# Performance work log

Hardware: AMD Instinct MI355X
Metric: run time of the kernel (lower is better)

Reference implementation:

```python
import jax, jax.numpy as jnp
import numpy as np

NPOINT = 1024
RADIUS = 0.2
NSAMPLE = 32


def furthest_point_sampling(xyz, npoint):
    # xyz: (B, N, 3) -> (B, npoint) int32 indices
    B, N, _ = xyz.shape

    def step(carry, _):
        dist, far = carry
        centroid = jnp.take_along_axis(xyz, far[:, None, None], axis=1)  # (B,1,3)
        d = jnp.sum((xyz - centroid) ** 2, axis=-1)                       # (B,N)
        dist = jnp.minimum(dist, d)
        new_far = jnp.argmax(dist, axis=-1).astype(jnp.int32)
        return (dist, new_far), far

    init = (jnp.full((B, N), 1e10, xyz.dtype), jnp.zeros((B,), jnp.int32))
    _, idx = jax.lax.scan(step, init, None, length=npoint)
    return idx.T  # (B, npoint)


def ball_query(xyz, new_xyz, radius, nsample):
    # xyz: (B,N,3), new_xyz: (B,S,3) -> (B,S,nsample) int32 indices
    N = xyz.shape[1]
    d2 = jnp.sum((new_xyz[:, :, None, :] - xyz[:, None, :, :]) ** 2, axis=-1)  # (B,S,N)
    # pick first `nsample` indices within radius (CUDA ball_query semantics)
    key = jnp.where(d2 < radius * radius, jnp.arange(N, dtype=jnp.int32)[None, None, :], N)
    idx = jnp.sort(key, axis=-1)[..., :nsample]          # (B,S,nsample)
    first = idx[..., :1]
    idx = jnp.where(idx == N, first, idx)                # pad with first valid
    return jnp.clip(idx, 0, N - 1).astype(jnp.int32)     # guard empty balls


def sa_forward(xyz, features, W1, s1, b1, W2, s2, b2, W3, s3, b3):
    B, N, _ = xyz.shape
    center_idx = furthest_point_sampling(xyz, NPOINT)                     # (B,S)
    new_xyz = jnp.take_along_axis(xyz, center_idx[..., None], axis=1)     # (B,S,3)

    idx = ball_query(xyz, new_xyz, RADIUS, NSAMPLE)                       # (B,S,K)
    # group xyz (relative coords) and features
    g_xyz = jnp.take_along_axis(xyz[:, None], idx[..., None], axis=2)     # (B,S,K,3)
    g_xyz = g_xyz - new_xyz[:, :, None, :]
    feats_n = jnp.swapaxes(features, 1, 2)                                # (B,N,C)
    g_feat = jnp.take_along_axis(feats_n[:, None], idx[..., None], axis=2)  # (B,S,K,C)
    g = jnp.concatenate([g_xyz, g_feat], axis=-1)                         # (B,S,K,3+C)
    x = jnp.transpose(g, (0, 3, 1, 2))                                    # (B,3+C,S,K)

    # 1x1 conv MLP with (folded) BN affine + ReLU
    for W, s, b in ((W1, s1, b1), (W2, s2, b2), (W3, s3, b3)):
        x = jax.nn.relu(jnp.einsum('oi,bisk->bosk', W, x)
                        * s[None, :, None, None] + b[None, :, None, None])
    new_features = jnp.max(x, axis=-1)                                    # (B,Cout,S)
    return new_xyz, new_features


def setup_inputs() -> dict:
    key = jax.random.key(0)
    ks = jax.random.split(key, 11)
    B, N, C = 4, 16384, 64
    return {
        'xyz': jax.random.uniform(ks[0], (B, N, 3), jnp.float32),
        'features': jax.random.normal(ks[1], (B, C, N), jnp.float32),
        'W1': jax.random.normal(ks[2], (64, C + 3), jnp.float32) * 0.1,
        's1': jax.random.uniform(ks[3], (64,), jnp.float32),
        'b1': jax.random.normal(ks[4], (64,), jnp.float32) * 0.1,
        'W2': jax.random.normal(ks[5], (64, 64), jnp.float32) * 0.1,
        's2': jax.random.uniform(ks[6], (64,), jnp.float32),
        'b2': jax.random.normal(ks[7], (64,), jnp.float32) * 0.1,
        'W3': jax.random.normal(ks[8], (128, 64), jnp.float32) * 0.1,
        's3': jax.random.uniform(ks[9], (128,), jnp.float32),
        'b3': jax.random.normal(ks[10], (128,), jnp.float32) * 0.1,
    }


def reference(xyz, features, W1, s1, b1, W2, s2, b2, W3, s3, b3):
    return sa_forward(xyz, features, W1, s1, b1, W2, s2, b2, W3, s3, b3)
```

## Files before the change

kernel.cpp:

```cpp
#include <hip/hip_runtime.h>
#include <cstdint>
#include <cstddef>

#define BATCH   4
#define NPTS    16384
#define NPOINT  1024
#define NSAMPLE 32
#define CIN     67
#define R2f     0.04f

__global__ __launch_bounds__(1024) void fps_kernel(
    const float* __restrict__ xyz, float* __restrict__ out_newxyz)
{
  const int b = blockIdx.x;
  const float* base = xyz + (size_t)b * NPTS * 3;
  const int t = threadIdx.x;
  const int lane = t & 63, wid = t >> 6;

  float px[16], py[16], pz[16], dist[16];
#pragma unroll
  for (int j = 0; j < 16; ++j) {
    int p = t + (j << 10);
    px[j] = base[p * 3 + 0];
    py[j] = base[p * 3 + 1];
    pz[j] = base[p * 3 + 2];
    dist[j] = 1e10f;
  }

  __shared__ float s_v[16];
  __shared__ int   s_i[16];
  __shared__ int   s_far;

  int far = 0;
  float cx = base[0], cy = base[1], cz = base[2];

  for (int it = 0; it < NPOINT; ++it) {
    if (t == 0) {
      int o = (b * NPOINT + it) * 3;
      out_newxyz[o + 0] = cx;
      out_newxyz[o + 1] = cy;
      out_newxyz[o + 2] = cz;
    }
    float bv = -1.0f; int bi = 0x7fffffff;
#pragma unroll
    for (int j = 0; j < 16; ++j) {
      float dx = __fsub_rn(px[j], cx);
      float dy = __fsub_rn(py[j], cy);
      float dz = __fsub_rn(pz[j], cz);
      float d  = __fadd_rn(__fadd_rn(__fmul_rn(dx, dx), __fmul_rn(dy, dy)),
                           __fmul_rn(dz, dz));
      float nd = fminf(dist[j], d);
      dist[j] = nd;
      bool tk = nd > bv;
      bv = tk ? nd : bv;
      bi = tk ? (t + (j << 10)) : bi;
    }
#pragma unroll
    for (int off = 32; off >= 1; off >>= 1) {
      float ov = __shfl_xor(bv, off);
      int   oi = __shfl_xor(bi, off);
      bool tk = (ov > bv) || (ov == bv && oi < bi);
      bv = tk ? ov : bv;
      bi = tk ? oi : bi;
    }
    if (lane == 0) { s_v[wid] = bv; s_i[wid] = bi; }
    __syncthreads();
    if (wid == 0) {
      float v = (lane < 16) ? s_v[lane] : -1.0f;
      int   i = (lane < 16) ? s_i[lane] : 0x7fffffff;
#pragma unroll
      for (int off = 8; off >= 1; off >>= 1) {
        float ov = __shfl_xor(v, off);
        int   oi = __shfl_xor(i, off);
        bool tk = (ov > v) || (ov == v && oi < i);
        v = tk ? ov : v;
        i = tk ? oi : i;
      }
      if (lane == 0) s_far = i;
    }
    __syncthreads();
    far = s_far;
    cx = base[far * 3 + 0];
    cy = base[far * 3 + 1];
    cz = base[far * 3 + 2];
  }
}

__global__ __launch_bounds__(256) void transpose_kernel(
    const float* __restrict__ f, float* __restrict__ ft)
{
  __shared__ float tile[64][65];
  int b  = blockIdx.x >> 8;
  int n0 = (blockIdx.x & 255) << 6;
  for (int v = threadIdx.x; v < 64 * 64; v += 256) {
    int c = v >> 6, j = v & 63;
    tile[c][j] = f[((size_t)(b * 64 + c)) * NPTS + n0 + j];
  }
  __syncthreads();
  for (int v = threadIdx.x; v < 64 * 64; v += 256) {
    int j = v >> 6, c = v & 63;
    ft[((size_t)(b * NPTS + n0 + j)) * 64 + c] = tile[c][j];
  }
}

__global__ __launch_bounds__(1024) void mlp_kernel(
    const float* __restrict__ xyz,
    const float* __restrict__ feats,
    const float* __restrict__ featsT,
    const float* __restrict__ nx,
    const float* __restrict__ W1, const float* __restrict__ s1, const float* __restrict__ b1,
    const float* __restrict__ W2, const float* __restrict__ s2, const float* __restrict__ b2,
    const float* __restrict__ W3, const float* __restrict__ s3, const float* __restrict__ b3,
    float* __restrict__ outF)
{
  __shared__ float W1t[CIN * 64];
  __shared__ float W2t[64 * 64];
  __shared__ float sb[512];
  __shared__ float xs[CIN * 34];
  __shared__ float h1[64 * 34];
  __shared__ float h2[64 * 34];
  __shared__ int   hm[128];
  __shared__ int   lid8[8][NSAMPLE];

  const int tid = threadIdx.x;
  const int lane = tid & 63, w = tid >> 6;

  for (int v = tid; v < CIN * 64; v += 1024) {
    int o = v / CIN, i = v - o * CIN;
    W1t[i * 64 + o] = W1[v];
  }
  for (int v = tid; v < 64 * 64; v += 1024) {
    int o = v >> 6, i = v & 63;
    W2t[i * 64 + o] = W2[v];
  }
  if (tid < 64)       sb[tid]       = s1[tid];
  else if (tid < 128) sb[tid]       = b1[tid - 64];
  else if (tid < 192) sb[tid]       = s2[tid - 128];
  else if (tid < 256) sb[tid]       = b2[tid - 192];
  else if (tid < 384) sb[tid]       = s3[tid - 256];
  else if (tid < 512) sb[tid]       = b3[tid - 384];

  if (w < 8) {
    int g = (blockIdx.x << 3) + w;
    int b = g >> 10;
    const float* base = xyz + (size_t)b * NPTS * 3;
    float cx = nx[g * 3 + 0], cy = nx[g * 3 + 1], cz = nx[g * 3 + 2];
    int cnt = 0, fidx = -1;
    for (int c0 = 0; c0 < NPTS && cnt < NSAMPLE; c0 += 64) {
      int i = c0 + lane;
      float dx = __fsub_rn(base[i * 3 + 0], cx);
      float dy = __fsub_rn(base[i * 3 + 1], cy);
      float dz = __fsub_rn(base[i * 3 + 2], cz);
      float d2 = __fadd_rn(__fadd_rn(__fmul_rn(dx, dx), __fmul_rn(dy, dy)),
                           __fmul_rn(dz, dz));
      bool pred = d2 < R2f;
      unsigned long long mk = __ballot(pred);
      if (pred) {
        int rank = cnt + __popcll(mk & ((1ull << lane) - 1ull));
        if (rank < NSAMPLE) lid8[w][rank] = i;
        if (rank == 0) fidx = i;
      }
      cnt += __popcll(mk);
    }
#pragma unroll
    for (int off = 32; off >= 1; off >>= 1) {
      int o = __shfl_xor(fidx, off);
      fidx = o > fidx ? o : fidx;
    }
    if (lane >= cnt && lane < NSAMPLE) lid8[w][lane] = fidx;
  }
  __syncthreads();

  for (int ci = 0; ci < 8; ++ci) {
    int g = (blockIdx.x << 3) + ci;
    int b = g >> 10, m = g & 1023;

    {
      int k = tid >> 5, c0 = tid & 31;
      int id = lid8[ci][k];
      for (int c = c0; c < CIN; c += 32) {
        float val;
        if (c < 3)
          val = __fsub_rn(xyz[((size_t)b * NPTS + id) * 3 + c], nx[g * 3 + c]);
        else if (featsT)
          val = featsT[((size_t)b * NPTS + id) * 64 + (c - 3)];
        else
          val = feats[((size_t)(b * 64 + (c - 3))) * NPTS + id];
        xs[c * 34 + k] = val;
      }
      if (tid < 128) hm[tid] = 0;
    }
    __syncthreads();

    {
      int oc = tid & 63, k0 = (tid >> 6) << 1;
      float a0 = 0.f, a1 = 0.f;
#pragma unroll 4
      for (int i = 0; i < CIN; ++i) {
        float ww = W1t[i * 64 + oc];
        a0 = fmaf(ww, xs[i * 34 + k0], a0);
        a1 = fmaf(ww, xs[i * 34 + k0 + 1], a1);
      }
      float s = sb[oc], bb = sb[64 + oc];
      h1[oc * 34 + k0]     = fmaxf(fmaf(a0, s, bb), 0.f);
      h1[oc * 34 + k0 + 1] = fmaxf(fmaf(a1, s, bb), 0.f);
    }
    __syncthreads();

    {
      int oc = tid & 63, k0 = (tid >> 6) << 1;
      float a0 = 0.f, a1 = 0.f;
#pragma unroll 4
      for (int i = 0; i < 64; ++i) {
        float ww = W2t[i * 64 + oc];
        a0 = fmaf(ww, h1[i * 34 + k0], a0);
        a1 = fmaf(ww, h1[i * 34 + k0 + 1], a1);
      }
      float s = sb[128 + oc], bb = sb[192 + oc];
      h2[oc * 34 + k0]     = fmaxf(fmaf(a0, s, bb), 0.f);
      h2[oc * 34 + k0 + 1] = fmaxf(fmaf(a1, s, bb), 0.f);
    }
    __syncthreads();

    {
      int oc = tid & 127, k0 = (tid >> 7) << 2;
      const float4* W3v = reinterpret_cast<const float4*>(W3);
      float a0 = 0.f, a1 = 0.f, a2 = 0.f, a3 = 0.f;
#pragma unroll 4
      for (int i4 = 0; i4 < 16; ++i4) {
        float4 wv = W3v[oc * 16 + i4];
        const float* hr = &h2[(i4 * 4) * 34 + k0];
        a0 = fmaf(wv.x, hr[0], a0); a1 = fmaf(wv.x, hr[1], a1);
        a2 = fmaf(wv.x, hr[2], a2); a3 = fmaf(wv.x, hr[3], a3);
        hr += 34;
        a0 = fmaf(wv.y, hr[0], a0); a1 = fmaf(wv.y, hr[1], a1);
        a2 = fmaf(wv.y, hr[2], a2); a3 = fmaf(wv.y, hr[3], a3);
        hr += 34;
        a0 = fmaf(wv.z, hr[0], a0); a1 = fmaf(wv.z, hr[1], a1);
        a2 = fmaf(wv.z, hr[2], a2); a3 = fmaf(wv.z, hr[3], a3);
        hr += 34;
        a0 = fmaf(wv.w, hr[0], a0); a1 = fmaf(wv.w, hr[1], a1);
        a2 = fmaf(wv.w, hr[2], a2); a3 = fmaf(wv.w, hr[3], a3);
      }
      float s = sb[256 + oc], bb = sb[384 + oc];
      float v0 = fmaxf(fmaf(a0, s, bb), 0.f);
      float v1 = fmaxf(fmaf(a1, s, bb), 0.f);
      float v2 = fmaxf(fmaf(a2, s, bb), 0.f);
      float v3 = fmaxf(fmaf(a3, s, bb), 0.f);
      float mv = fmaxf(fmaxf(v0, v1), fmaxf(v2, v3));
      atomicMax(&hm[oc], __float_as_int(mv));
    }
    __syncthreads();

    if (tid < 128)
      outF[(((size_t)b * 128 + tid) << 10) + m] = __int_as_float(hm[tid]);
    __syncthreads();
  }
}

extern "C" void kernel_launch(void* const* d_in, const int* in_sizes, int n_in,
                              void* d_out, int out_size, void* d_ws, size_t ws_size,
                              hipStream_t stream)
{
  if (n_in < 11) return;
  const float* xyz   = (const float*)d_in[0];
  const float* feats = (const float*)d_in[1];
  const float* W1 = (const float*)d_in[2];
  const float* s1 = (const float*)d_in[3];
  const float* b1 = (const float*)d_in[4];
  const float* W2 = (const float*)d_in[5];
  const float* s2 = (const float*)d_in[6];
  const float* b2 = (const float*)d_in[7];
  const float* W3 = (const float*)d_in[8];
  const float* s3 = (const float*)d_in[9];
  const float* b3 = (const float*)d_in[10];
  float* out = (float*)d_out;

  float* featsT = nullptr;
  size_t needT = (size_t)BATCH * NPTS * 64 * sizeof(float);
  if (ws_size >= needT) featsT = (float*)d_ws;

  fps_kernel<<<BATCH, 1024, 0, stream>>>(xyz, out);
  if (featsT) transpose_kernel<<<BATCH * 256, 256, 0, stream>>>(feats, featsT);
  mlp_kernel<<<512, 1024, 0, stream>>>(xyz, feats, featsT, out,
                                       W1, s1, b1, W2, s2, b2, W3, s3, b3,
                                       out + BATCH * NPOINT * 3);
}
```

Baseline: 2.549 ms.

## Use DPP reductions and one barrier per FPS iteration with 512 threads

Restructures the furthest-point-sampling kernel to use 512 threads with 32 points each. The per-iteration argmax reduction now uses DPP row shifts and row broadcasts instead of shuffle XOR. The second shared-memory barrier is removed by double-buffering the per-wave partials by iteration parity, with every wave reducing the 8 partials redundantly and using readfirstlane. This targets the latency of the 1024 serial FPS iterations, at the cost of more per-thread work and higher register pressure.

```diff
diff --git a/kernel.cpp b/kernel.cpp
--- a/kernel.cpp
+++ b/kernel.cpp
@@ -9,29 +9,41 @@
 #define CIN     67
 #define R2f     0.04f
 
-__global__ __launch_bounds__(1024) void fps_kernel(
+#define FPS_T   512
+#define FPS_P   32
+
+template <int CTRL, int RMASK>
+__device__ __forceinline__ void amax_dpp(float& v, int& i) {
+  int nv = __builtin_amdgcn_update_dpp(__float_as_int(v), __float_as_int(v),
+                                       CTRL, RMASK, 0xf, false);
+  int ni = __builtin_amdgcn_update_dpp(i, i, CTRL, RMASK, 0xf, false);
+  float fv = __int_as_float(nv);
+  bool tk = (fv > v) || (fv == v && ni < i);
+  v = tk ? fv : v;
+  i = tk ? ni : i;
+}
+
+__global__ __launch_bounds__(512) void fps_kernel(
     const float* __restrict__ xyz, float* __restrict__ out_newxyz)
 {
   const int b = blockIdx.x;
   const float* base = xyz + (size_t)b * NPTS * 3;
   const int t = threadIdx.x;
-  const int lane = t & 63, wid = t >> 6;
-
-  float px[16], py[16], pz[16], dist[16];
+  const int lane = t & 63, w = t >> 6;
+
+  float px[FPS_P], py[FPS_P], pz[FPS_P], dist[FPS_P];
 #pragma unroll
-  for (int j = 0; j < 16; ++j) {
-    int p = t + (j << 10);
+  for (int j = 0; j < FPS_P; ++j) {
+    int p = t + (j << 9);
     px[j] = base[p * 3 + 0];
     py[j] = base[p * 3 + 1];
     pz[j] = base[p * 3 + 2];
     dist[j] = 1e10f;
   }
 
-  __shared__ float s_v[16];
-  __shared__ int   s_i[16];
-  __shared__ int   s_far;
-
-  int far = 0;
+  __shared__ float s_wv[2][8];
+  __shared__ int   s_wi[2][8];
+
   float cx = base[0], cy = base[1], cz = base[2];
 
   for (int it = 0; it < NPOINT; ++it) {
@@ -43,7 +55,7 @@
     }
     float bv = -1.0f; int bi = 0x7fffffff;
 #pragma unroll
-    for (int j = 0; j < 16; ++j) {
+    for (int j = 0; j < FPS_P; ++j) {
       float dx = __fsub_rn(px[j], cx);
       float dy = __fsub_rn(py[j], cy);
       float dz = __fsub_rn(pz[j], cz);
@@ -53,33 +65,26 @@
       dist[j] = nd;
       bool tk = nd > bv;
       bv = tk ? nd : bv;
-      bi = tk ? (t + (j << 10)) : bi;
-    }
-#pragma unroll
-    for (int off = 32; off >= 1; off >>= 1) {
-      float ov = __shfl_xor(bv, off);
-      int   oi = __shfl_xor(bi, off);
-      bool tk = (ov > bv) || (ov == bv && oi < bi);
-      bv = tk ? ov : bv;
-      bi = tk ? oi : bi;
-    }
-    if (lane == 0) { s_v[wid] = bv; s_i[wid] = bi; }
-    __syncthreads();
-    if (wid == 0) {
-      float v = (lane < 16) ? s_v[lane] : -1.0f;
-      int   i = (lane < 16) ? s_i[lane] : 0x7fffffff;
-#pragma unroll
-      for (int off = 8; off >= 1; off >>= 1) {
-        float ov = __shfl_xor(v, off);
-        int   oi = __shfl_xor(i, off);
-        bool tk = (ov > v) || (ov == v && oi < i);
-        v = tk ? ov : v;
-        i = tk ? oi : i;
-      }
-      if (lane == 0) s_far = i;
-    }
-    __syncthreads();
-    far = s_far;
+      bi = tk ? (t + (j << 9)) : bi;
+    }
+    amax_dpp<0x121, 0xf>(bv, bi);
+    amax_dpp<0x122, 0xf>(bv, bi);
+    amax_dpp<0x124, 0xf>(bv, bi);
+    amax_dpp<0x128, 0xf>(bv, bi);
+    amax_dpp<0x142, 0xa>(bv, bi);
+    amax_dpp<0x143, 0xc>(bv, bi);
+
+    const int par = it & 1;
+    if (lane == 63) { s_wv[par][w] = bv; s_wi[par][w] = bi; }
+    __syncthreads();
+
+    float gv = s_wv[par][lane & 7];
+    int   gi = s_wi[par][lane & 7];
+    amax_dpp<0x121, 0xf>(gv, gi);
+    amax_dpp<0x122, 0xf>(gv, gi);
+    amax_dpp<0x124, 0xf>(gv, gi);
+
+    int far = __builtin_amdgcn_readfirstlane(gi);
     cx = base[far * 3 + 0];
     cy = base[far * 3 + 1];
     cz = base[far * 3 + 2];
@@ -280,7 +285,7 @@
   size_t needT = (size_t)BATCH * NPTS * 64 * sizeof(float);
   if (ws_size >= needT) featsT = (float*)d_ws;
 
-  fps_kernel<<<BATCH, 1024, 0, stream>>>(xyz, out);
+  fps_kernel<<<BATCH, FPS_T, 0, stream>>>(xyz, out);
   if (featsT) transpose_kernel<<<BATCH * 256, 256, 0, stream>>>(feats, featsT);
   mlp_kernel<<<512, 1024, 0, stream>>>(xyz, feats, featsT, out,
                                        W1, s1, b1, W2, s2, b2, W3, s3, b3,
```

New measurement: 2.261 ms. 1.13x faster.
